# Performance work log

Hardware: AMD Instinct MI355X
Metric: run time of the kernel (lower is better)

## Reference

```python
import jax, jax.numpy as jnp
import numpy as np

N = 100000
IN_DIM = 256
HID = 256
EMB = 64
E = 3200000
EPS = 1e-3  # keras BatchNormalization default epsilon


def setup_inputs() -> dict:
    key = jax.random.key(0)
    ks = jax.random.split(key, 8)
    x = jax.random.normal(ks[0], (N, IN_DIM), dtype=jnp.float32)
    edge_row = jax.random.randint(ks[1], (E,), 0, N, dtype=jnp.int32)
    edge_col = jax.random.randint(ks[2], (E,), 0, N, dtype=jnp.int32)
    edge_val = jax.random.uniform(ks[3], (E,), dtype=jnp.float32)
    # glorot-uniform weights
    lim1 = float(np.sqrt(6.0 / (IN_DIM + HID)))
    w1 = jax.random.uniform(ks[4], (IN_DIM, HID), minval=-lim1, maxval=lim1, dtype=jnp.float32)
    lim2 = float(np.sqrt(6.0 / (HID + EMB)))
    w2 = jax.random.uniform(ks[5], (HID, EMB), minval=-lim2, maxval=lim2, dtype=jnp.float32)
    # BN params (inference mode uses moving stats)
    gamma1 = jnp.ones((HID,), jnp.float32)
    beta1 = jnp.zeros((HID,), jnp.float32)
    mean1 = jax.random.normal(ks[6], (HID,), dtype=jnp.float32) * 0.1
    var1 = jnp.ones((HID,), jnp.float32)
    gamma2 = jnp.ones((EMB,), jnp.float32)
    beta2 = jnp.zeros((EMB,), jnp.float32)
    mean2 = jax.random.normal(ks[7], (EMB,), dtype=jnp.float32) * 0.1
    var2 = jnp.ones((EMB,), jnp.float32)
    return dict(x=x, edge_row=edge_row, edge_col=edge_col, edge_val=edge_val,
                w1=w1, w2=w2, gamma1=gamma1, beta1=beta1, mean1=mean1, var1=var1,
                gamma2=gamma2, beta2=beta2, mean2=mean2, var2=var2)


def _spmm(edge_row, edge_col, edge_val, dense):
    # out[i] = sum_{e: row_e == i} val_e * dense[col_e]
    gathered = edge_val[:, None] * dense[edge_col]  # [E, D]
    return jax.ops.segment_sum(gathered, edge_row, num_segments=N)


def _bn_inf(h, gamma, beta, mean, var):
    return (h - mean) * jax.lax.rsqrt(var + EPS) * gamma + beta


def reference(x, edge_row, edge_col, edge_val, w1, w2,
              gamma1, beta1, mean1, var1, gamma2, beta2, mean2, var2):
    # layer 1: A @ (X W1), BN (inference), ReLU; dropout is identity at inference
    h = _spmm(edge_row, edge_col, edge_val, x @ w1)
    h = jax.nn.relu(_bn_inf(h, gamma1, beta1, mean1, var1))
    # layer 2
    z = _spmm(edge_row, edge_col, edge_val, h @ w2)
    z = _bn_inf(z, gamma2, beta2, mean2, var2)
    return z
```

## Files before the change

kernel.cpp:

```cpp
#include <hip/hip_runtime.h>
#include <hip/hip_bf16.h>

constexpr int NN   = 100000;
constexpr int IND  = 256;
constexpr int HIDD = 256;
constexpr int EMBD = 64;
constexpr int EE   = 3200000;
constexpr int CB    = 8;
constexpr int NB    = ((NN - 1) >> CB) + 1;
constexpr int NBP   = 512;
constexpr int CHUNK = 4096;
constexpr int EPT   = CHUNK / 256;
constexpr int NCHUNK = (EE + CHUNK - 1) / CHUNK;
constexpr int GMT    = 8;
constexpr int GROWS  = GMT * 16;
constexpr int GGRID  = (NN + GROWS - 1) / GROWS;
constexpr int APITCH = 264;
#define EPS_BN 1e-3f

typedef short  short8  __attribute__((ext_vector_type(8)));
typedef float  floatx4 __attribute__((ext_vector_type(4)));
typedef float  floatx2 __attribute__((ext_vector_type(2)));

static __device__ __forceinline__ unsigned short f2bf(float f) {
  __hip_bfloat16 b = __float2bfloat16(f);
  union { __hip_bfloat16 b; unsigned short u; } cv;
  cv.b = b;
  return cv.u;
}
static __device__ __forceinline__ float bf2f(unsigned short u) {
  return __uint_as_float(((unsigned)u) << 16);
}
static __device__ __forceinline__ unsigned char f2fp8(float f) {
  return (unsigned char)__builtin_amdgcn_cvt_pk_fp8_f32(f, f, 0, false);
}

__global__ __launch_bounds__(256) void swz_w1_kernel(
    const float* __restrict__ w1, unsigned short* __restrict__ w1s) {
  const int t = blockIdx.x * blockDim.x + threadIdx.x;
  const int lane = t & 63;
  const int f = t >> 6;
  const int kt = f >> 4;
  const int nt = f & 15;
  const int n = nt * 16 + (lane & 15);
#pragma unroll
  for (int j = 0; j < 8; ++j) {
    const int k = kt * 32 + (lane >> 4) * 8 + j;
    w1s[(size_t)(f * 64 + lane) * 8 + j] = f2bf(w1[k * HIDD + n]);
  }
}

__global__ __launch_bounds__(256) void swz_w2_kernel(
    const float* __restrict__ w2, unsigned short* __restrict__ w2s) {
  const int t = blockIdx.x * blockDim.x + threadIdx.x;
  const int lane = t & 63;
  const int f = t >> 6;
  const int kt = f >> 2;
  const int nt = f & 3;
  const int n = nt * 16 + (lane & 15);
#pragma unroll
  for (int j = 0; j < 8; ++j) {
    const int k = kt * 32 + (lane >> 4) * 8 + j;
    w2s[(size_t)(f * 64 + lane) * 8 + j] = f2bf(w2[k * EMBD + n]);
  }
}

__global__ __launch_bounds__(512) void gemm1_mfma(
    const float* __restrict__ x, const unsigned short* __restrict__ w1s,
    unsigned char* __restrict__ h0) {
  __shared__ unsigned short sa[2][16][APITCH];
  const int tid  = threadIdx.x;
  const int lane = tid & 63;
  const int wave = tid >> 6;
  const int quad = lane >> 4;
  const int l15  = lane & 15;
  const short8* w1v = (const short8*)w1s;
  short8 bf[2][8];
#pragma unroll
  for (int nt2 = 0; nt2 < 2; ++nt2)
#pragma unroll
    for (int kt = 0; kt < 8; ++kt)
      bf[nt2][kt] = w1v[(size_t)(kt * 16 + wave * 2 + nt2) * 64 + lane];

  const int mbase = blockIdx.x * GROWS;
  const int srow = tid >> 5;
  const int scol = (tid & 31) * 8;

  auto srcp = [&](int mt) -> const float* {
    int r = mbase + mt * 16 + srow;
    if (r >= NN) r = NN - 1;
    return x + (size_t)r * IND + scol;
  };

  {
    const float* p = srcp(0);
    float4 g0 = *(const float4*)(p);
    float4 g1 = *(const float4*)(p + 4);
    short8 s;
    s[0] = (short)f2bf(g0.x); s[1] = (short)f2bf(g0.y);
    s[2] = (short)f2bf(g0.z); s[3] = (short)f2bf(g0.w);
    s[4] = (short)f2bf(g1.x); s[5] = (short)f2bf(g1.y);
    s[6] = (short)f2bf(g1.z); s[7] = (short)f2bf(g1.w);
    *(short8*)&sa[0][srow][(tid & 31) * 8] = s;
  }

#pragma unroll
  for (int mt = 0; mt < GMT; ++mt) {
    const int cur = mt & 1;
    float4 g0, g1;
    if (mt + 1 < GMT) {
      const float* p = srcp(mt + 1);
      g0 = *(const float4*)(p);
      g1 = *(const float4*)(p + 4);
    }
    __syncthreads();
    floatx4 c0 = {0.f, 0.f, 0.f, 0.f};
    floatx4 c1 = {0.f, 0.f, 0.f, 0.f};
#pragma unroll
    for (int kt = 0; kt < 8; ++kt) {
      short8 a = *(const short8*)&sa[cur][l15][quad * 8 + kt * 32];
      c0 = __builtin_amdgcn_mfma_f32_16x16x32_bf16(a, bf[0][kt], c0, 0, 0, 0);
      c1 = __builtin_amdgcn_mfma_f32_16x16x32_bf16(a, bf[1][kt], c1, 0, 0, 0);
    }
    const int m0 = mbase + mt * 16;
    if (m0 < NN) {
      unsigned char* o = h0 + (size_t)(m0 + quad * 4) * HIDD + wave * 32 + l15;
#pragma unroll
      for (int r = 0; r < 4; ++r) {
        o[(size_t)r * HIDD]      = f2fp8(c0[r]);
        o[(size_t)r * HIDD + 16] = f2fp8(c1[r]);
      }
    }
    if (mt + 1 < GMT) {
      short8 s;
      s[0] = (short)f2bf(g0.x); s[1] = (short)f2bf(g0.y);
      s[2] = (short)f2bf(g0.z); s[3] = (short)f2bf(g0.w);
      s[4] = (short)f2bf(g1.x); s[5] = (short)f2bf(g1.y);
      s[6] = (short)f2bf(g1.z); s[7] = (short)f2bf(g1.w);
      *(short8*)&sa[cur ^ 1][srow][(tid & 31) * 8] = s;
    }
  }
}

__global__ __launch_bounds__(256) void gemm2_mfma(
    const unsigned short* __restrict__ hb, const unsigned short* __restrict__ w2s,
    unsigned char* __restrict__ z0) {
  __shared__ unsigned short sa[2][16][APITCH];
  const int tid  = threadIdx.x;
  const int lane = tid & 63;
  const int wave = tid >> 6;
  const int quad = lane >> 4;
  const int l15  = lane & 15;
  const short8* w2v = (const short8*)w2s;
  short8 bf[8];
#pragma unroll
  for (int kt = 0; kt < 8; ++kt)
    bf[kt] = w2v[(size_t)(kt * 4 + wave) * 64 + lane];

  const int mbase = blockIdx.x * GROWS;
  const int srow = tid >> 4;
  const int scol = (tid & 15) * 16;

  auto srcp = [&](int mt) -> const unsigned short* {
    int r = mbase + mt * 16 + srow;
    if (r >= NN) r = NN - 1;
    return hb + (size_t)r * HIDD + scol;
  };

  {
    const unsigned short* p = srcp(0);
    short8 g0 = *(const short8*)(p);
    short8 g1 = *(const short8*)(p + 8);
    *(short8*)&sa[0][srow][scol]     = g0;
    *(short8*)&sa[0][srow][scol + 8] = g1;
  }

#pragma unroll
  for (int mt = 0; mt < GMT; ++mt) {
    const int cur = mt & 1;
    short8 g0, g1;
    if (mt + 1 < GMT) {
      const unsigned short* p = srcp(mt + 1);
      g0 = *(const short8*)(p);
      g1 = *(const short8*)(p + 8);
    }
    __syncthreads();
    floatx4 c = {0.f, 0.f, 0.f, 0.f};
#pragma unroll
    for (int kt = 0; kt < 8; ++kt) {
      short8 a = *(const short8*)&sa[cur][l15][quad * 8 + kt * 32];
      c = __builtin_amdgcn_mfma_f32_16x16x32_bf16(a, bf[kt], c, 0, 0, 0);
    }
    const int m0 = mbase + mt * 16;
    if (m0 < NN) {
      unsigned char* o = z0 + (size_t)(m0 + quad * 4) * EMBD + wave * 16 + l15;
#pragma unroll
      for (int r = 0; r < 4; ++r) o[(size_t)r * EMBD] = f2fp8(c[r]);
    }
    if (mt + 1 < GMT) {
      *(short8*)&sa[cur ^ 1][srow][scol]     = g0;
      *(short8*)&sa[cur ^ 1][srow][scol + 8] = g1;
    }
  }
}

__global__ __launch_bounds__(256) void histb_kernel(
    const int* __restrict__ row, int* __restrict__ bcnt) {
  __shared__ int lcnt[NB];
  for (int i = threadIdx.x; i < NB; i += 256) lcnt[i] = 0;
  __syncthreads();
  const int base = blockIdx.x * CHUNK;
  const int lim  = min(EE - base, CHUNK);
  for (int i = threadIdx.x; i < lim; i += 256)
    atomicAdd(&lcnt[row[base + i] >> CB], 1);
  __syncthreads();
  for (int i = threadIdx.x; i < NB; i += 256) {
    const int c = lcnt[i];
    if (c) atomicAdd(&bcnt[i * 16], c);
  }
}

__global__ __launch_bounds__(512) void bscan_kernel(
    const int* __restrict__ bcnt, int* __restrict__ bucket_start,
    int* __restrict__ bcur) {
  __shared__ int lds[512];
  int v = (threadIdx.x < NB) ? bcnt[threadIdx.x * 16] : 0;
  lds[threadIdx.x] = v;
  for (int off = 1; off < 512; off <<= 1) {
    __syncthreads();
    int t = (threadIdx.x >= off) ? lds[threadIdx.x - off] : 0;
    __syncthreads();
    lds[threadIdx.x] += t;
  }
  __syncthreads();
  if (threadIdx.x < NB) {
    const int excl = lds[threadIdx.x] - v;
    bucket_start[threadIdx.x] = excl;
    bcur[threadIdx.x * 16] = excl;
  }
  if (threadIdx.x == 0) bucket_start[NB] = EE;
}

__global__ __launch_bounds__(256) void partA_kernel(
    const int* __restrict__ row, const int* __restrict__ col,
    const float* __restrict__ val, int* __restrict__ bcur,
    unsigned long long* __restrict__ staged) {
  __shared__ unsigned long long sbuf[CHUNK];
  __shared__ int cnt[NBP];
  __shared__ int scn[NBP];
  __shared__ int cur[NB];
  __shared__ int gofs[NB];
  const int base = blockIdx.x * CHUNK;
  const int lim  = min(EE - base, CHUNK);
  for (int i = threadIdx.x; i < NBP; i += 256) cnt[i] = 0;
  __syncthreads();
  unsigned long long rec[EPT];
  int bkt[EPT];
#pragma unroll
  for (int j = 0; j < EPT; ++j) {
    const int idx = threadIdx.x + j * 256;
    bkt[j] = -1;
    if (idx < lim) {
      const int e = base + idx;
      const int r = row[e];
      const int c = col[e];
      const unsigned short v = f2bf(val[e]);
      rec[j] = ((unsigned long long)r << 33) | ((unsigned long long)c << 16) | v;
      bkt[j] = r >> CB;
      atomicAdd(&cnt[bkt[j]], 1);
    }
  }
  __syncthreads();
  for (int i = threadIdx.x; i < NBP; i += 256) scn[i] = cnt[i];
  __syncthreads();
  for (int off = 1; off < NBP; off <<= 1) {
    const int i0 = threadIdx.x, i1 = threadIdx.x + 256;
    const int t0 = (i0 >= off) ? scn[i0 - off] : 0;
    const int t1 = (i1 >= off) ? scn[i1 - off] : 0;
    __syncthreads();
    scn[i0] += t0;
    scn[i1] += t1;
    __syncthreads();
  }
  for (int b = threadIdx.x; b < NB; b += 256) cur[b] = scn[b] - cnt[b];
  __syncthreads();
#pragma unroll
  for (int j = 0; j < EPT; ++j)
    if (bkt[j] >= 0) {
      const int p = atomicAdd(&cur[bkt[j]], 1);
      sbuf[p] = rec[j];
    }
  __syncthreads();
  for (int b = threadIdx.x; b < NB; b += 256) {
    const int c = cnt[b];
    const int g = (c > 0) ? atomicAdd(&bcur[b * 16], c) : 0;
    gofs[b] = g - (scn[b] - c);
  }
  __syncthreads();
  for (int s = threadIdx.x; s < lim; s += 256) {
    const unsigned long long rc = sbuf[s];
    const int b = (int)(rc >> (33 + CB));
    staged[(size_t)(gofs[b] + s)] = rc;
  }
}

__global__ __launch_bounds__(256) void partB_kernel(
    const int* __restrict__ bucket_start,
    const unsigned long long* __restrict__ staged,
    int2* __restrict__ edges, int* __restrict__ row_start) {
  __shared__ int cnt[1 << CB];
  __shared__ int ofs[1 << CB];
  const int b  = blockIdx.x;
  const int r0 = b << CB;
  const int rn = min(NN - r0, 1 << CB);
  const int s  = bucket_start[b];
  const int e  = bucket_start[b + 1];
  cnt[threadIdx.x] = 0;
  __syncthreads();
  const unsigned* hi = (const unsigned*)staged;
  for (int p = s + threadIdx.x; p < e; p += 256) {
    const unsigned hw = hi[2 * p + 1];
    const int r = (int)((hw >> 1) & 0x1FFFF);
    atomicAdd(&cnt[r - r0], 1);
  }
  __syncthreads();
  const int v = cnt[threadIdx.x];
  ofs[threadIdx.x] = v;
  for (int off = 1; off < 256; off <<= 1) {
    __syncthreads();
    const int t = (threadIdx.x >= off) ? ofs[threadIdx.x - off] : 0;
    __syncthreads();
    ofs[threadIdx.x] += t;
  }
  __syncthreads();
  const int excl = ofs[threadIdx.x] - v;
  if ((int)threadIdx.x < rn) row_start[r0 + threadIdx.x] = s + excl;
  if (b == NB - 1 && threadIdx.x == 0) row_start[NN] = e;
  __syncthreads();
  cnt[threadIdx.x] = s + excl;
  __syncthreads();
  for (int p = s + threadIdx.x; p < e; p += 256) {
    const unsigned long long rc = staged[p];
    const int r = (int)(rc >> 33);
    const int c = (int)((rc >> 16) & 0x1FFFF);
    const float vv = bf2f((unsigned short)(rc & 0xFFFF));
    const int q = atomicAdd(&cnt[r - r0], 1);
    int2 pk; pk.x = c << 6; pk.y = __float_as_int(vv);
    edges[q] = pk;
  }
}

__global__ __launch_bounds__(256) void spmm1_kernel(
    const unsigned char* __restrict__ h0, const int* __restrict__ row_start,
    const int2* __restrict__ edges,
    const float* __restrict__ gamma, const float* __restrict__ beta,
    const float* __restrict__ mean, const float* __restrict__ var,
    unsigned short* __restrict__ h) {
  const int row  = (blockIdx.x * blockDim.x + threadIdx.x) >> 6;
  const int lane = threadIdx.x & 63;
  const int lane4 = lane * 4;
  const int s = row_start[row];
  const int e = row_start[row + 1];
  floatx2 acc01 = {0.f, 0.f};
  floatx2 acc23 = {0.f, 0.f};
  int p = s;
  for (; p + 8 <= e; p += 8) {
    int2 er[8];
    unsigned gg[8];
#pragma unroll
    for (int j = 0; j < 8; ++j) er[j] = edges[p + j];
#pragma unroll
    for (int j = 0; j < 8; ++j)
      gg[j] = *(const unsigned*)(h0 + ((size_t)(unsigned)er[j].x * 4) + lane4);
#pragma unroll
    for (int j = 0; j < 8; ++j) {
      const float v = __int_as_float(er[j].y);
      floatx2 lo = __builtin_amdgcn_cvt_pk_f32_fp8(gg[j], false);
      floatx2 hi = __builtin_amdgcn_cvt_pk_f32_fp8(gg[j], true);
      acc01 += lo * v;
      acc23 += hi * v;
    }
  }
  for (; p < e; ++p) {
    int2 e0 = edges[p];
    unsigned g0 = *(const unsigned*)(h0 + ((size_t)(unsigned)e0.x * 4) + lane4);
    const float v0 = __int_as_float(e0.y);
    floatx2 lo = __builtin_amdgcn_cvt_pk_f32_fp8(g0, false);
    floatx2 hi = __builtin_amdgcn_cvt_pk_f32_fp8(g0, true);
    acc01 += lo * v0;
    acc23 += hi * v0;
  }
  const int d = lane4;
  float4 g = *(const float4*)(gamma + d);
  float4 b = *(const float4*)(beta + d);
  float4 m = *(const float4*)(mean + d);
  float4 vv = *(const float4*)(var + d);
  ushort4 o;
  o.x = f2bf(fmaxf(fmaf((acc01.x - m.x) * rsqrtf(vv.x + EPS_BN), g.x, b.x), 0.f));
  o.y = f2bf(fmaxf(fmaf((acc01.y - m.y) * rsqrtf(vv.y + EPS_BN), g.y, b.y), 0.f));
  o.z = f2bf(fmaxf(fmaf((acc23.x - m.z) * rsqrtf(vv.z + EPS_BN), g.z, b.z), 0.f));
  o.w = f2bf(fmaxf(fmaf((acc23.y - m.w) * rsqrtf(vv.w + EPS_BN), g.w, b.w), 0.f));
  *(ushort4*)(h + (size_t)row * HIDD + d) = o;
}

__global__ __launch_bounds__(256) void spmm2_kernel(
    const unsigned char* __restrict__ z0, const int* __restrict__ row_start,
    const int2* __restrict__ edges,
    const float* __restrict__ gamma, const float* __restrict__ beta,
    const float* __restrict__ mean, const float* __restrict__ var,
    float* __restrict__ out) {
  const int row  = (blockIdx.x * blockDim.x + threadIdx.x) >> 6;
  const int lane = threadIdx.x & 63;
  const int s = row_start[row];
  const int e = row_start[row + 1];
  float acc = 0.f;
  int p = s;
  for (; p + 8 <= e; p += 8) {
    int2 er[8];
    unsigned char gb[8];
#pragma unroll
    for (int j = 0; j < 8; ++j) er[j] = edges[p + j];
#pragma unroll
    for (int j = 0; j < 8; ++j)
      gb[j] = z0[(size_t)(unsigned)er[j].x + lane];
#pragma unroll
    for (int j = 0; j < 8; ++j)
      acc = fmaf(__int_as_float(er[j].y),
                 __builtin_amdgcn_cvt_f32_fp8((int)gb[j], 0), acc);
  }
  for (; p < e; ++p) {
    int2 e0 = edges[p];
    unsigned char g0 = z0[(size_t)(unsigned)e0.x + lane];
    acc = fmaf(__int_as_float(e0.y), __builtin_amdgcn_cvt_f32_fp8((int)g0, 0), acc);
  }
  float r = fmaf((acc - mean[lane]) * rsqrtf(var[lane] + EPS_BN), gamma[lane],
                 beta[lane]);
  out[(size_t)row * EMBD + lane] = r;
}

extern "C" void kernel_launch(void* const* d_in, const int* in_sizes, int n_in,
                              void* d_out, int out_size, void* d_ws, size_t ws_size,
                              hipStream_t stream) {
  const float* x        = (const float*)d_in[0];
  const int*   edge_row = (const int*)d_in[1];
  const int*   edge_col = (const int*)d_in[2];
  const float* edge_val = (const float*)d_in[3];
  const float* w1       = (const float*)d_in[4];
  const float* w2       = (const float*)d_in[5];
  const float* gamma1   = (const float*)d_in[6];
  const float* beta1    = (const float*)d_in[7];
  const float* mean1    = (const float*)d_in[8];
  const float* var1     = (const float*)d_in[9];
  const float* gamma2   = (const float*)d_in[10];
  const float* beta2    = (const float*)d_in[11];
  const float* mean2    = (const float*)d_in[12];
  const float* var2     = (const float*)d_in[13];
  float* out = (float*)d_out;

  char* ws = (char*)d_ws;
  size_t off = 0;
  auto alloc = [&](size_t bytes) -> void* {
    void* p = ws + off;
    off = (off + bytes + 255) & ~(size_t)255;
    return p;
  };
  unsigned char*  h0  = (unsigned char*)alloc((size_t)NN * HIDD);
  unsigned short* h   = (unsigned short*)alloc((size_t)NN * HIDD * 2);
  unsigned long long* staged = (unsigned long long*)h;
  unsigned char*  z0  = (unsigned char*)alloc((size_t)NN * EMBD);
  unsigned short* w1s = (unsigned short*)alloc((size_t)IND * HIDD * 2);
  unsigned short* w2s = (unsigned short*)alloc((size_t)HIDD * EMBD * 2);
  int*   row_start    = (int*)alloc((size_t)(NN + 1) * 4);
  int*   bcnt         = (int*)alloc((size_t)NB * 16 * 4);
  int*   bcur         = (int*)alloc((size_t)NB * 16 * 4);
  int*   bucket_start = (int*)alloc((size_t)(NB + 1) * 4);
  int2*  edges        = (int2*)alloc((size_t)EE * 8);

  swz_w1_kernel<<<8192 / 256, 256, 0, stream>>>(w1, w1s);
  swz_w2_kernel<<<2048 / 256, 256, 0, stream>>>(w2, w2s);

  hipMemsetAsync(bcnt, 0, (size_t)NB * 16 * 4, stream);
  histb_kernel<<<NCHUNK, 256, 0, stream>>>(edge_row, bcnt);
  bscan_kernel<<<1, 512, 0, stream>>>(bcnt, bucket_start, bcur);
  partA_kernel<<<NCHUNK, 256, 0, stream>>>(
      edge_row, edge_col, edge_val, bcur, staged);
  partB_kernel<<<NB, 256, 0, stream>>>(bucket_start, staged, edges, row_start);

  gemm1_mfma<<<GGRID, 512, 0, stream>>>(x, w1s, h0);
  spmm1_kernel<<<NN / 4, 256, 0, stream>>>(h0, row_start, edges,
                                           gamma1, beta1, mean1, var1, h);
  gemm2_mfma<<<GGRID, 256, 0, stream>>>(h, w2s, z0);
  spmm2_kernel<<<NN / 4, 256, 0, stream>>>(z0, row_start, edges,
                                           gamma2, beta2, mean2, var2, out);
}
```

Measured before the change: 545.6 us.

## Split each wavefront into four edge groups with wider gathers in SpMM kernels

Both SpMM kernels now split each 64-lane wavefront into four 16-lane groups, each handling a different edge, so a wavefront processes four edges at once with 16-byte (layer 1) or 4-byte (layer 2) fp8 gathers per lane. The partial sums are combined with cross-group shuffles, then each lane picks its output slice before applying BN. The aim is fewer, wider memory requests and more edges in flight, at the cost of extra registers, shuffle reductions and masked work on rows whose edge count is not a multiple of 16. Launch bounds now also request 8 blocks per SM.

```diff
diff --git a/kernel.cpp b/kernel.cpp
--- a/kernel.cpp
+++ b/kernel.cpp
@@ -350,7 +350,7 @@
   }
 }
 
-__global__ __launch_bounds__(256) void spmm1_kernel(
+__global__ __launch_bounds__(256, 8) void spmm1_kernel(
     const unsigned char* __restrict__ h0, const int* __restrict__ row_start,
     const int2* __restrict__ edges,
     const float* __restrict__ gamma, const float* __restrict__ beta,
@@ -358,52 +358,72 @@
     unsigned short* __restrict__ h) {
   const int row  = (blockIdx.x * blockDim.x + threadIdx.x) >> 6;
   const int lane = threadIdx.x & 63;
-  const int lane4 = lane * 4;
+  const int grp  = lane >> 4;
+  const int t    = lane & 15;
+  const int t16  = t * 16;
   const int s = row_start[row];
   const int e = row_start[row + 1];
-  floatx2 acc01 = {0.f, 0.f};
-  floatx2 acc23 = {0.f, 0.f};
-  int p = s;
-  for (; p + 8 <= e; p += 8) {
-    int2 er[8];
-    unsigned gg[8];
-#pragma unroll
-    for (int j = 0; j < 8; ++j) er[j] = edges[p + j];
-#pragma unroll
-    for (int j = 0; j < 8; ++j)
-      gg[j] = *(const unsigned*)(h0 + ((size_t)(unsigned)er[j].x * 4) + lane4);
-#pragma unroll
-    for (int j = 0; j < 8; ++j) {
-      const float v = __int_as_float(er[j].y);
-      floatx2 lo = __builtin_amdgcn_cvt_pk_f32_fp8(gg[j], false);
-      floatx2 hi = __builtin_amdgcn_cvt_pk_f32_fp8(gg[j], true);
-      acc01 += lo * v;
-      acc23 += hi * v;
-    }
-  }
-  for (; p < e; ++p) {
-    int2 e0 = edges[p];
-    unsigned g0 = *(const unsigned*)(h0 + ((size_t)(unsigned)e0.x * 4) + lane4);
-    const float v0 = __int_as_float(e0.y);
-    floatx2 lo = __builtin_amdgcn_cvt_pk_f32_fp8(g0, false);
-    floatx2 hi = __builtin_amdgcn_cvt_pk_f32_fp8(g0, true);
-    acc01 += lo * v0;
-    acc23 += hi * v0;
-  }
-  const int d = lane4;
-  float4 g = *(const float4*)(gamma + d);
-  float4 b = *(const float4*)(beta + d);
-  float4 m = *(const float4*)(mean + d);
+  floatx2 acc[8];
+#pragma unroll
+  for (int j = 0; j < 8; ++j) acc[j] = floatx2{0.f, 0.f};
+
+  for (int p = s; p < e; p += 16) {
+    unsigned coff[4];
+    float    vv4[4];
+#pragma unroll
+    for (int k = 0; k < 4; ++k) {
+      const int idx = p + k * 4 + grp;
+      const bool valid = idx < e;
+      const int2 er = edges[valid ? idx : e - 1];
+      coff[k] = valid ? (unsigned)er.x : 0u;
+      vv4[k]  = valid ? __int_as_float(er.y) : 0.f;
+    }
+    uint4 gg[4];
+#pragma unroll
+    for (int k = 0; k < 4; ++k)
+      gg[k] = *(const uint4*)(h0 + (size_t)coff[k] * 4 + t16);
+#pragma unroll
+    for (int k = 0; k < 4; ++k) {
+      const floatx2 v2 = {vv4[k], vv4[k]};
+      acc[0] += __builtin_amdgcn_cvt_pk_f32_fp8(gg[k].x, false) * v2;
+      acc[1] += __builtin_amdgcn_cvt_pk_f32_fp8(gg[k].x, true)  * v2;
+      acc[2] += __builtin_amdgcn_cvt_pk_f32_fp8(gg[k].y, false) * v2;
+      acc[3] += __builtin_amdgcn_cvt_pk_f32_fp8(gg[k].y, true)  * v2;
+      acc[4] += __builtin_amdgcn_cvt_pk_f32_fp8(gg[k].z, false) * v2;
+      acc[5] += __builtin_amdgcn_cvt_pk_f32_fp8(gg[k].z, true)  * v2;
+      acc[6] += __builtin_amdgcn_cvt_pk_f32_fp8(gg[k].w, false) * v2;
+      acc[7] += __builtin_amdgcn_cvt_pk_f32_fp8(gg[k].w, true)  * v2;
+    }
+  }
+#pragma unroll
+  for (int j = 0; j < 8; ++j) {
+    acc[j][0] += __shfl_xor(acc[j][0], 16);
+    acc[j][1] += __shfl_xor(acc[j][1], 16);
+  }
+#pragma unroll
+  for (int j = 0; j < 8; ++j) {
+    acc[j][0] += __shfl_xor(acc[j][0], 32);
+    acc[j][1] += __shfl_xor(acc[j][1], 32);
+  }
+  floatx2 pa, pb;
+  if (grp == 0)      { pa = acc[0]; pb = acc[1]; }
+  else if (grp == 1) { pa = acc[2]; pb = acc[3]; }
+  else if (grp == 2) { pa = acc[4]; pb = acc[5]; }
+  else               { pa = acc[6]; pb = acc[7]; }
+  const int d = t16 + grp * 4;
+  float4 g  = *(const float4*)(gamma + d);
+  float4 b  = *(const float4*)(beta + d);
+  float4 m  = *(const float4*)(mean + d);
   float4 vv = *(const float4*)(var + d);
   ushort4 o;
-  o.x = f2bf(fmaxf(fmaf((acc01.x - m.x) * rsqrtf(vv.x + EPS_BN), g.x, b.x), 0.f));
-  o.y = f2bf(fmaxf(fmaf((acc01.y - m.y) * rsqrtf(vv.y + EPS_BN), g.y, b.y), 0.f));
-  o.z = f2bf(fmaxf(fmaf((acc23.x - m.z) * rsqrtf(vv.z + EPS_BN), g.z, b.z), 0.f));
-  o.w = f2bf(fmaxf(fmaf((acc23.y - m.w) * rsqrtf(vv.w + EPS_BN), g.w, b.w), 0.f));
+  o.x = f2bf(fmaxf(fmaf((pa[0] - m.x) * rsqrtf(vv.x + EPS_BN), g.x, b.x), 0.f));
+  o.y = f2bf(fmaxf(fmaf((pa[1] - m.y) * rsqrtf(vv.y + EPS_BN), g.y, b.y), 0.f));
+  o.z = f2bf(fmaxf(fmaf((pb[0] - m.z) * rsqrtf(vv.z + EPS_BN), g.z, b.z), 0.f));
+  o.w = f2bf(fmaxf(fmaf((pb[1] - m.w) * rsqrtf(vv.w + EPS_BN), g.w, b.w), 0.f));
   *(ushort4*)(h + (size_t)row * HIDD + d) = o;
 }
 
-__global__ __launch_bounds__(256) void spmm2_kernel(
+__global__ __launch_bounds__(256, 8) void spmm2_kernel(
     const unsigned char* __restrict__ z0, const int* __restrict__ row_start,
     const int2* __restrict__ edges,
     const float* __restrict__ gamma, const float* __restrict__ beta,
@@ -411,31 +431,48 @@
     float* __restrict__ out) {
   const int row  = (blockIdx.x * blockDim.x + threadIdx.x) >> 6;
   const int lane = threadIdx.x & 63;
+  const int grp  = lane >> 4;
+  const int t    = lane & 15;
+  const int t4   = t * 4;
   const int s = row_start[row];
   const int e = row_start[row + 1];
-  float acc = 0.f;
-  int p = s;
-  for (; p + 8 <= e; p += 8) {
-    int2 er[8];
-    unsigned char gb[8];
-#pragma unroll
-    for (int j = 0; j < 8; ++j) er[j] = edges[p + j];
-#pragma unroll
-    for (int j = 0; j < 8; ++j)
-      gb[j] = z0[(size_t)(unsigned)er[j].x + lane];
-#pragma unroll
-    for (int j = 0; j < 8; ++j)
-      acc = fmaf(__int_as_float(er[j].y),
-                 __builtin_amdgcn_cvt_f32_fp8((int)gb[j], 0), acc);
-  }
-  for (; p < e; ++p) {
-    int2 e0 = edges[p];
-    unsigned char g0 = z0[(size_t)(unsigned)e0.x + lane];
-    acc = fmaf(__int_as_float(e0.y), __builtin_amdgcn_cvt_f32_fp8((int)g0, 0), acc);
-  }
-  float r = fmaf((acc - mean[lane]) * rsqrtf(var[lane] + EPS_BN), gamma[lane],
-                 beta[lane]);
-  out[(size_t)row * EMBD + lane] = r;
+  floatx2 a01 = {0.f, 0.f};
+  floatx2 a23 = {0.f, 0.f};
+  for (int p = s; p < e; p += 16) {
+    unsigned coff[4];
+    float    vv4[4];
+#pragma unroll
+    for (int k = 0; k < 4; ++k) {
+      const int idx = p + k * 4 + grp;
+      const bool valid = idx < e;
+      const int2 er = edges[valid ? idx : e - 1];
+      coff[k] = valid ? (unsigned)er.x : 0u;
+      vv4[k]  = valid ? __int_as_float(er.y) : 0.f;
+    }
+    unsigned gg[4];
+#pragma unroll
+    for (int k = 0; k < 4; ++k)
+      gg[k] = *(const unsigned*)(z0 + (size_t)coff[k] + t4);
+#pragma unroll
+    for (int k = 0; k < 4; ++k) {
+      const floatx2 v2 = {vv4[k], vv4[k]};
+      a01 += __builtin_amdgcn_cvt_pk_f32_fp8(gg[k], false) * v2;
+      a23 += __builtin_amdgcn_cvt_pk_f32_fp8(gg[k], true)  * v2;
+    }
+  }
+  a01[0] += __shfl_xor(a01[0], 16); a01[1] += __shfl_xor(a01[1], 16);
+  a23[0] += __shfl_xor(a23[0], 16); a23[1] += __shfl_xor(a23[1], 16);
+  a01[0] += __shfl_xor(a01[0], 32); a01[1] += __shfl_xor(a01[1], 32);
+  a23[0] += __shfl_xor(a23[0], 32); a23[1] += __shfl_xor(a23[1], 32);
+  float av;
+  if (grp == 0)      av = a01[0];
+  else if (grp == 1) av = a01[1];
+  else if (grp == 2) av = a23[0];
+  else               av = a23[1];
+  const int d = t4 + grp;
+  const float r = fmaf((av - mean[d]) * rsqrtf(var[d] + EPS_BN), gamma[d],
+                       beta[d]);
+  out[(size_t)row * EMBD + d] = r;
 }
 
 extern "C" void kernel_launch(void* const* d_in, const int* in_sizes, int n_in,
```

Measured after the change: 514.3 us. 5.7% less time.
